# Kernel optimization log

Hardware: AMD Instinct MI355X
Metric: run time of the kernel (lower is better)

Reference implementation:

```python
import jax, jax.numpy as jnp
import numpy as np
from jax import lax

LEAK = 0.2
GN_EPS = 1e-5
K_NEIGH = 16
GROUPS = 4


def knn_idx(coor_k, coor_q, k):
    # coor_k: [B,Nk,3], coor_q: [B,Nq,3] -> [B,Nq,k] indices of k nearest in coor_k
    d = (jnp.sum(coor_q * coor_q, -1, keepdims=True)
         - 2.0 * jnp.einsum('bqc,bkc->bqk', coor_q, coor_k)
         + jnp.sum(coor_k * coor_k, -1)[:, None, :])
    _, idx = lax.top_k(-d, k)
    return idx


def graph_feature(coor_q, x_q, coor_k, x_k, k):
    # coor_*: [B,3,N*]; x_q: [B,C,Nq]; x_k: [B,C,Nk] -> [B,2C,Nq,k]
    idx = knn_idx(lax.stop_gradient(coor_k).transpose(0, 2, 1),
                  lax.stop_gradient(coor_q).transpose(0, 2, 1), k)
    B = x_k.shape[0]
    x_k_t = x_k.transpose(0, 2, 1)                      # [B,Nk,C]
    b_idx = jnp.arange(B)[:, None, None]
    nb = x_k_t[b_idx, idx]                              # [B,Nq,k,C]
    nb = nb.transpose(0, 3, 1, 2)                       # [B,C,Nq,k]
    xq = x_q[:, :, :, None]                             # [B,C,Nq,1]
    return jnp.concatenate([nb - xq, jnp.broadcast_to(xq, nb.shape)], axis=1)


def conv_gn_lrelu_max(f, w, gamma, beta):
    # f: [B,Cin,N,k]; w: [Cout,Cin] -> [B,Cout,N] (max over k)
    y = jnp.einsum('oc,bcnk->bonk', w, f)
    B, C, N, Kk = y.shape
    g = y.reshape(B, GROUPS, C // GROUPS, N, Kk)
    mu = g.mean((2, 3, 4), keepdims=True)
    var = g.var((2, 3, 4), keepdims=True)
    g = (g - mu) * lax.rsqrt(var + GN_EPS)
    y = g.reshape(B, C, N, Kk) * gamma[None, :, None, None] + beta[None, :, None, None]
    y = jnp.where(y >= 0, y, LEAK * y)
    return y.max(axis=-1)


def fps(xyz, n):
    # xyz: [B,N,3] -> [B,n] int32 (furthest point sampling, start at index 0)
    B, N, _ = xyz.shape
    d0 = jnp.sum((xyz - xyz[:, :1]) ** 2, -1)           # dist to point 0
    def body(dist, _):
        idx = jnp.argmax(dist, -1)                       # [B]
        nxt = jnp.take_along_axis(xyz, idx[:, None, None], 1)
        dist = jnp.minimum(dist, jnp.sum((xyz - nxt) ** 2, -1))
        return dist, idx
    _, idxs = lax.scan(body, d0, None, length=n - 1)     # [n-1,B]
    first = jnp.zeros((1, B), idxs.dtype)
    return jnp.concatenate([first, idxs], 0).T           # [B,n]


def fps_downsample(coor, x, n):
    # coor: [B,3,N], x: [B,C,N] -> ([B,3,n], [B,C,n])
    idx = fps(lax.stop_gradient(coor).transpose(0, 2, 1), n)
    comb = jnp.concatenate([coor, x], axis=1)            # [B,3+C,N]
    b_idx = jnp.arange(coor.shape[0])[:, None]
    new = comb.transpose(0, 2, 1)[b_idx, idx].transpose(0, 2, 1)
    return new[:, :3], new[:, 3:]


def setup_inputs() -> dict:
    key = jax.random.key(0)
    ks = jax.random.split(key, 16)
    s = 0.1
    return {
        'x': jax.random.normal(ks[0], (32, 2048, 3), jnp.float32),
        'w_in': jax.random.normal(ks[1], (8, 3), jnp.float32) * s,
        'b_in': jnp.zeros((8,), jnp.float32),
        'w1': jax.random.normal(ks[2], (32, 16), jnp.float32) * s,
        'g1': jnp.ones((32,), jnp.float32), 'be1': jnp.zeros((32,), jnp.float32),
        'w2': jax.random.normal(ks[3], (64, 64), jnp.float32) * s,
        'g2': jnp.ones((64,), jnp.float32), 'be2': jnp.zeros((64,), jnp.float32),
        'w3': jax.random.normal(ks[4], (64, 128), jnp.float32) * s,
        'g3': jnp.ones((64,), jnp.float32), 'be3': jnp.zeros((64,), jnp.float32),
        'w4': jax.random.normal(ks[5], (256, 128), jnp.float32) * s,
        'g4': jnp.ones((256,), jnp.float32), 'be4': jnp.zeros((256,), jnp.float32),
        'num0': 512,
        'num1': 128,
    }


def reference(x, w_in, b_in, w1, g1, be1, w2, g2, be2, w3, g3, be3, w4, g4, be4, num0, num1):
    coor = x.transpose(0, 2, 1)                          # [B,3,N]
    f = jnp.einsum('oc,bcn->bon', w_in, coor) + b_in[None, :, None]  # input_trans
    f = graph_feature(coor, f, coor, f, K_NEIGH)         # [B,16,N,k]
    f = conv_gn_lrelu_max(f, w1, g1, be1)                # [B,32,N]
    coor_q, f_q = fps_downsample(coor, f, num0)
    f = graph_feature(coor_q, f_q, coor, f, K_NEIGH)     # [B,64,num0,k]
    f = conv_gn_lrelu_max(f, w2, g2, be2)                # [B,64,num0]
    coor = coor_q
    f = graph_feature(coor, f, coor, f, K_NEIGH)         # [B,128,num0,k]
    f = conv_gn_lrelu_max(f, w3, g3, be3)                # [B,64,num0]
    coor_q, f_q = fps_downsample(coor, f, num1)
    f = graph_feature(coor_q, f_q, coor, f, K_NEIGH)     # [B,128,num1,k]
    f = conv_gn_lrelu_max(f, w4, g4, be4)                # [B,256,num1]
    coor = coor_q
    return coor.transpose(0, 2, 1), f.transpose(0, 2, 1)  # [B,num1,3], [B,num1,256]
```

## Files before the change

kernel.cpp:

```cpp
#include <hip/hip_runtime.h>

#define BB 32
#define NPTS0 2048
#define KNB 16
#define KC 256

constexpr int ilog2c(int n){ int l=0; while(n>1){ n>>=1; ++l; } return l; }

static __device__ __forceinline__ float sq3(float a, float b, float c){
  return __fadd_rn(__fadd_rn(__fmul_rn(a,a),__fmul_rn(b,b)),__fmul_rn(c,c));
}

template<int CTRL, int RM>
static __device__ __forceinline__ float dpp_maxf(float v){
  int s = __builtin_amdgcn_update_dpp(__float_as_int(v), __float_as_int(v), CTRL, RM, 0xF, false);
  return fmaxf(v, __int_as_float(s));
}
template<int CTRL, int RM>
static __device__ __forceinline__ unsigned dpp_minu(unsigned v){
  unsigned s = (unsigned)__builtin_amdgcn_update_dpp((int)v, (int)v, CTRL, RM, 0xF, false);
  return s < v ? s : v;
}

static __device__ __forceinline__ void proj_body(const float* __restrict__ x,
    const float* __restrict__ w, const float* __restrict__ bias, float* __restrict__ f0,
    int blk)
{
  int gid = blk*256 + threadIdx.x;
  if (gid >= BB*NPTS0) return;
  float x0 = x[gid*3+0], x1 = x[gid*3+1], x2 = x[gid*3+2];
  #pragma unroll
  for (int o = 0; o < 8; ++o){
    float acc = __fmul_rn(w[o*3+0], x0);
    acc = __fmaf_rn(w[o*3+1], x1, acc);
    acc = __fmaf_rn(w[o*3+2], x2, acc);
    f0[gid*8+o] = __fadd_rn(acc, bias[o]);
  }
}

#define KDECL(I) float th##I = __builtin_inff(); int ti##I = 0;
#define KINS(I,J) if (th##I < th##J){ float tv=th##I; th##I=th##J; th##J=tv; \
                                      int tj=ti##I; ti##I=ti##J; ti##J=tj; }
#define KCASCADE KINS(15,14) KINS(14,13) KINS(13,12) KINS(12,11) KINS(11,10) \
  KINS(10,9) KINS(9,8) KINS(8,7) KINS(7,6) KINS(6,5) KINS(5,4) KINS(4,3) \
  KINS(3,2) KINS(2,1) KINS(1,0)
#define KST(I) pd[base+I] = th##I; pi[base+I] = (unsigned char)ti##I;
#define MST(I) oidx[obase+I] = ti##I;

static __device__ __forceinline__ void knn_part_body(const float* __restrict__ qpts,
    const float* __restrict__ kpts, int Nq, int Nk, int nkc,
    float* __restrict__ pd, unsigned char* __restrict__ pi,
    int b, int qcb, int kc, float4* kk4)
{
  int tid = threadIdx.x;
  {
    int j = kc*KC + tid;
    float a = kpts[(b*Nk+j)*3+0];
    float c = kpts[(b*Nk+j)*3+1];
    float d = kpts[(b*Nk+j)*3+2];
    kk4[tid] = make_float4(a, c, d, sq3(a,c,d));
  }
  __syncthreads();
  int q = qcb*256 + tid;
  if (q >= Nq) return;
  float qx = qpts[(b*Nq+q)*3+0], qy = qpts[(b*Nq+q)*3+1], qz = qpts[(b*Nq+q)*3+2];
  float qq = sq3(qx,qy,qz);
  KDECL(0) KDECL(1) KDECL(2) KDECL(3) KDECL(4) KDECL(5) KDECL(6) KDECL(7)
  KDECL(8) KDECL(9) KDECL(10) KDECL(11) KDECL(12) KDECL(13) KDECL(14) KDECL(15)
  for (int j=0;j<KC;j++){
    float4 k4 = kk4[j];
    float dot = __fmul_rn(qx,k4.x);
    dot = __fmaf_rn(qy,k4.y,dot);
    dot = __fmaf_rn(qz,k4.z,dot);
    float d = __fadd_rn(__fsub_rn(qq, __fmul_rn(2.0f,dot)), k4.w);
    if (d < th15){
      th15 = d; ti15 = j;
      KCASCADE
    }
  }
  size_t base = ((size_t)(b*Nq+q)*nkc + kc)*KNB;
  KST(0) KST(1) KST(2) KST(3) KST(4) KST(5) KST(6) KST(7)
  KST(8) KST(9) KST(10) KST(11) KST(12) KST(13) KST(14) KST(15)
}

static __device__ __forceinline__ void knn_merge_body(const float* __restrict__ pd,
    const unsigned char* __restrict__ pi, int Nq, int nkc, int* __restrict__ oidx,
    int blk)
{
  int gid = blk*256 + threadIdx.x;
  if (gid >= BB*Nq) return;
  KDECL(0) KDECL(1) KDECL(2) KDECL(3) KDECL(4) KDECL(5) KDECL(6) KDECL(7)
  KDECL(8) KDECL(9) KDECL(10) KDECL(11) KDECL(12) KDECL(13) KDECL(14) KDECL(15)
  size_t base = (size_t)gid*nkc*KNB;
  for (int kc=0;kc<nkc;kc++){
    size_t cb = base + (size_t)kc*KNB;
    for (int i=0;i<KNB;i++){
      float d = pd[cb+i];
      if (d >= th15) break;
      int j = kc*KC + (int)pi[cb+i];
      th15 = d; ti15 = j;
      KCASCADE
    }
  }
  int obase = gid*KNB;
  MST(0) MST(1) MST(2) MST(3) MST(4) MST(5) MST(6) MST(7)
  MST(8) MST(9) MST(10) MST(11) MST(12) MST(13) MST(14) MST(15)
}

#define FPS_LOAD(T) float px##T, py##T, pz##T, d##T; { int i_=T*256+tid; \
  px##T=P[i_*3+0]; py##T=P[i_*3+1]; pz##T=P[i_*3+2]; \
  float dx_=__fsub_rn(px##T,c0x), dy_=__fsub_rn(py##T,c0y), dz_=__fsub_rn(pz##T,c0z); \
  d##T=sq3(dx_,dy_,dz_); bm=fmaxf(bm,d##T); }
#define FPS_MATCH(T) if (d##T == m_w) ci = (unsigned)(T*256 + tid);
#define FPS_OWN(T) if ((idx_w>>8) == T##u){ cx=px##T; cy=py##T; cz=pz##T; }
#define FPS_UPD(T) { float dx_=__fsub_rn(px##T,sx), dy_=__fsub_rn(py##T,sy), dz_=__fsub_rn(pz##T,sz); \
  float nd_=sq3(dx_,dy_,dz_); d##T=fminf(d##T,nd_); nbm=fmaxf(nbm,d##T); }

#define FPS_REDUCE_AND_PICK \
    float v = bm; \
    v = dpp_maxf<0x111, 0xF>(v); \
    v = dpp_maxf<0x112, 0xF>(v); \
    v = dpp_maxf<0x114, 0xF>(v); \
    v = dpp_maxf<0x118, 0xF>(v); \
    v = dpp_maxf<0x142, 0xA>(v); \
    v = dpp_maxf<0x143, 0xC>(v); \
    float m_w = __int_as_float(__builtin_amdgcn_readlane(__float_as_int(v), 63)); \
    unsigned ci = 0xFFFFFFFFu;

#define FPS_MIN_AND_MERGE \
    ci = dpp_minu<0x111, 0xF>(ci); \
    ci = dpp_minu<0x112, 0xF>(ci); \
    ci = dpp_minu<0x114, 0xF>(ci); \
    ci = dpp_minu<0x118, 0xF>(ci); \
    ci = dpp_minu<0x142, 0xA>(ci); \
    ci = dpp_minu<0x143, 0xC>(ci); \
    unsigned idx_w = (unsigned)__builtin_amdgcn_readlane((int)ci, 63); \
    int par = s & 1;

#define FPS_CROSSWAVE \
    __syncthreads(); \
    float4 q0 = *(const float4*)&swp[par][0][0]; float z0 = swp[par][0][4]; \
    float4 q1 = *(const float4*)&swp[par][1][0]; float z1 = swp[par][1][4]; \
    float4 q2 = *(const float4*)&swp[par][2][0]; float z2 = swp[par][2][4]; \
    float4 q3 = *(const float4*)&swp[par][3][0]; float z3 = swp[par][3][4]; \
    float mm = q0.x; unsigned mi = __float_as_uint(q0.y); \
    float sx = q0.z, sy = q0.w, sz = z0; \
    if (q1.x > mm || (q1.x == mm && __float_as_uint(q1.y) < mi)){ \
      mm = q1.x; mi = __float_as_uint(q1.y); sx = q1.z; sy = q1.w; sz = z1; } \
    if (q2.x > mm || (q2.x == mm && __float_as_uint(q2.y) < mi)){ \
      mm = q2.x; mi = __float_as_uint(q2.y); sx = q2.z; sy = q2.w; sz = z2; } \
    if (q3.x > mm || (q3.x == mm && __float_as_uint(q3.y) < mi)){ \
      mm = q3.x; mi = __float_as_uint(q3.y); sx = q3.z; sy = q3.w; sz = z3; } \
    if (tid == 0) oibuf[s] = (int)mi;

static __device__ __forceinline__ void fps8_body(const float* __restrict__ pts,
    int S, int* __restrict__ oidx, int b, char* smraw)
{
  float (*swp)[4][8] = reinterpret_cast<float(*)[4][8]>(smraw);
  int* oibuf = reinterpret_cast<int*>(smraw + 256);
  int tid = threadIdx.x, wid = tid >> 6;
  const float* P = pts + (size_t)b*2048*3;
  float c0x = P[0], c0y = P[1], c0z = P[2];
  float bm = -1.0f;
  FPS_LOAD(0) FPS_LOAD(1) FPS_LOAD(2) FPS_LOAD(3)
  FPS_LOAD(4) FPS_LOAD(5) FPS_LOAD(6) FPS_LOAD(7)
  if (tid == 0) oibuf[0] = 0;
  for (int s=1; s<S; ++s){
    FPS_REDUCE_AND_PICK
    FPS_MATCH(7) FPS_MATCH(6) FPS_MATCH(5) FPS_MATCH(4)
    FPS_MATCH(3) FPS_MATCH(2) FPS_MATCH(1) FPS_MATCH(0)
    FPS_MIN_AND_MERGE
    if (tid == (int)(idx_w & 255u)){
      float cx = px0, cy = py0, cz = pz0;
      FPS_OWN(1) FPS_OWN(2) FPS_OWN(3) FPS_OWN(4) FPS_OWN(5) FPS_OWN(6) FPS_OWN(7)
      float4* wp = (float4*)&swp[par][wid][0];
      *wp = make_float4(m_w, __uint_as_float(idx_w), cx, cy);
      swp[par][wid][4] = cz;
    }
    FPS_CROSSWAVE
    float nbm = -1.0f;
    FPS_UPD(0) FPS_UPD(1) FPS_UPD(2) FPS_UPD(3)
    FPS_UPD(4) FPS_UPD(5) FPS_UPD(6) FPS_UPD(7)
    bm = nbm;
  }
  __syncthreads();
  for (int s2 = tid; s2 < S; s2 += 256) oidx[b*S + s2] = oibuf[s2];
}

static __device__ __forceinline__ void fps2_body(const float* __restrict__ pts,
    int S, int* __restrict__ oidx, int b, char* smraw)
{
  float (*swp)[4][8] = reinterpret_cast<float(*)[4][8]>(smraw);
  int* oibuf = reinterpret_cast<int*>(smraw + 256);
  int tid = threadIdx.x, wid = tid >> 6;
  const float* P = pts + (size_t)b*512*3;
  float c0x = P[0], c0y = P[1], c0z = P[2];
  float bm = -1.0f;
  FPS_LOAD(0) FPS_LOAD(1)
  if (tid == 0) oibuf[0] = 0;
  for (int s=1; s<S; ++s){
    FPS_REDUCE_AND_PICK
    FPS_MATCH(1) FPS_MATCH(0)
    FPS_MIN_AND_MERGE
    if (tid == (int)(idx_w & 255u)){
      float cx = px0, cy = py0, cz = pz0;
      FPS_OWN(1)
      float4* wp = (float4*)&swp[par][wid][0];
      *wp = make_float4(m_w, __uint_as_float(idx_w), cx, cy);
      swp[par][wid][4] = cz;
    }
    FPS_CROSSWAVE
    float nbm = -1.0f;
    FPS_UPD(0) FPS_UPD(1)
    bm = nbm;
  }
  __syncthreads();
  for (int s2 = tid; s2 < S; s2 += 256) oidx[b*S + s2] = oibuf[s2];
}

__global__ __launch_bounds__(256) void fused1_kernel(const float* __restrict__ x,
    const float* __restrict__ w_in, const float* __restrict__ b_in,
    float* __restrict__ f0, float* __restrict__ pd1, unsigned char* __restrict__ pi1,
    int* __restrict__ fidx0)
{
  __shared__ __align__(16) char sm[4096];
  int bid = blockIdx.x;
  if (bid < 32){
    __builtin_amdgcn_s_setprio(3);
    fps8_body(x, 512, fidx0, bid, sm);
  } else if (bid < 32+2048){
    int r = bid - 32;
    int b = r & 31; int rest = r >> 5;
    knn_part_body(x, x, 2048, 2048, 8, pd1, pi1, b, rest & 7, rest >> 3, (float4*)sm);
  } else {
    proj_body(x, w_in, b_in, f0, bid - 2080);
  }
}

__global__ __launch_bounds__(256) void fused2_kernel(const float* __restrict__ coorq1,
    const float* __restrict__ x,
    float* __restrict__ pd2, unsigned char* __restrict__ pi2,
    float* __restrict__ pd3, unsigned char* __restrict__ pi3,
    int* __restrict__ fidx1,
    const float* __restrict__ pd1, const unsigned char* __restrict__ pi1,
    int* __restrict__ idx1)
{
  __shared__ __align__(16) char sm[4096];
  int bid = blockIdx.x;
  if (bid < 32){
    __builtin_amdgcn_s_setprio(3);
    fps2_body(coorq1, 128, fidx1, bid, sm);
  } else if (bid < 32+512){
    int r = bid - 32;
    int b = r & 31; int rest = r >> 5;
    knn_part_body(coorq1, x, 512, 2048, 8, pd2, pi2, b, rest & 1, rest >> 1, (float4*)sm);
  } else if (bid < 32+512+128){
    int r = bid - 544;
    int b = r & 31; int rest = r >> 5;
    knn_part_body(coorq1, coorq1, 512, 512, 2, pd3, pi3, b, rest & 1, rest >> 1, (float4*)sm);
  } else {
    knn_merge_body(pd1, pi1, 2048, 8, idx1, bid - 672);
  }
}

__global__ __launch_bounds__(256) void knn_part_kernel(const float* __restrict__ qpts,
    const float* __restrict__ kpts, int Nq, int Nk,
    float* __restrict__ pd, unsigned char* __restrict__ pi)
{
  __shared__ __align__(16) float4 kk4[KC];
  knn_part_body(qpts, kpts, Nq, Nk, gridDim.z, pd, pi,
                blockIdx.x, blockIdx.y, blockIdx.z, kk4);
}

__global__ __launch_bounds__(256) void knn_merge_kernel(const float* __restrict__ pd,
    const unsigned char* __restrict__ pi, int Nq, int nkc, int* __restrict__ oidx)
{
  knn_merge_body(pd, pi, Nq, nkc, oidx, blockIdx.x);
}

template<int C, int O, bool DIFF>
static __device__ __forceinline__ void gemv_body(const float* __restrict__ fin,
    const float* __restrict__ W, float* __restrict__ out, int Npts, int blk)
{
  constexpr int NT = O/8;
  constexpr int LNT = ilog2c(NT);
  int gid = blk*256 + threadIdx.x;
  if (gid >= BB*Npts*NT) return;
  int tile = gid & (NT-1);
  int pn = gid >> LNT;
  const float* frow = fin + pn*C;
  float f[C];
  #pragma unroll
  for (int c=0;c<C;c++) f[c] = frow[c];
  float acc[8];
  const float* wbase = W + (tile*8)*(2*C);
  #pragma unroll
  for (int oo=0;oo<8;oo++){
    const float* wrow = wbase + oo*(2*C);
    float a = 0.f;
    #pragma unroll
    for (int c=0;c<C;c++){
      float wv = DIFF ? __fsub_rn(wrow[C+c], wrow[c]) : wrow[c];
      a = __fmaf_rn(wv, f[c], a);
    }
    acc[oo] = a;
  }
  float* orow = out + pn*O + tile*8;
  #pragma unroll
  for (int oo=0;oo<8;oo++) orow[oo] = acc[oo];
}

template<int C, int O>
__global__ __launch_bounds__(256) void gemv_dual_kernel(const float* __restrict__ finA,
    const float* __restrict__ finB, const float* __restrict__ W,
    float* __restrict__ outA, float* __restrict__ outB,
    int NptsA, int NptsB, int nAblk)
{
  int bid = blockIdx.x;
  if (bid < nAblk) gemv_body<C,O,false>(finA, W, outA, NptsA, bid);
  else             gemv_body<C,O,true >(finB, W, outB, NptsB, bid - nAblk);
}

template<int O>
__global__ __launch_bounds__(256) void stats2_kernel(const float* __restrict__ A,
    const float* __restrict__ Bq, const int* __restrict__ idx, int Nq, int Nk,
    double* __restrict__ part)
{
  constexpr int O4 = O/4;
  int b = blockIdx.x, split = blockIdx.y, nsplit = gridDim.y;
  int qlen = Nq / nsplit, q0 = split*qlen;
  int tid = threadIdx.x;
  int pairs = qlen * KNB;
  double s1[4] = {0.0,0.0,0.0,0.0};
  double s2[4] = {0.0,0.0,0.0,0.0};
  for (int p = tid; p < pairs; p += 256){
    int q = q0 + (p >> 4);
    int kk = p & 15;
    int j = idx[(b*Nq+q)*KNB + kk];
    const float* arow = A + (size_t)(b*Nk+j)*O;
    const float* brow = Bq + (size_t)(b*Nq+q)*O;
    #pragma unroll
    for (int g=0; g<4; ++g){
      float cs1 = 0.f, cs2 = 0.f;
      #pragma unroll
      for (int c=0; c<O4; c+=4){
        float4 a4 = *(const float4*)(arow + g*O4 + c);
        float4 b4 = *(const float4*)(brow + g*O4 + c);
        float y0 = a4.x+b4.x, y1 = a4.y+b4.y, y2 = a4.z+b4.z, y3 = a4.w+b4.w;
        cs1 += ((y0+y1)+(y2+y3));
        cs2 = fmaf(y0,y0,cs2); cs2 = fmaf(y1,y1,cs2);
        cs2 = fmaf(y2,y2,cs2); cs2 = fmaf(y3,y3,cs2);
      }
      s1[g] += (double)cs1;
      s2[g] += (double)cs2;
    }
  }
  #pragma unroll
  for (int m=32;m>0;m>>=1){
    #pragma unroll
    for (int g=0; g<4; ++g){
      s1[g] += __shfl_down(s1[g], m);
      s2[g] += __shfl_down(s2[g], m);
    }
  }
  __shared__ double sh[4][8];
  int lane = tid & 63, w = tid >> 6;
  if (lane == 0){
    #pragma unroll
    for (int g=0; g<4; ++g){ sh[w][g*2] = s1[g]; sh[w][g*2+1] = s2[g]; }
  }
  __syncthreads();
  if (tid == 0){
    #pragma unroll
    for (int g=0; g<4; ++g){
      double t1 = (sh[0][g*2]+sh[1][g*2]) + (sh[2][g*2]+sh[3][g*2]);
      double t2 = (sh[0][g*2+1]+sh[1][g*2+1]) + (sh[2][g*2+1]+sh[3][g*2+1]);
      int pi = (b*4+g)*nsplit + split;
      part[pi*2] = t1; part[pi*2+1] = t2;
    }
  }
}

template<int O>
__global__ __launch_bounds__(256) void final_kernel(const float* __restrict__ A,
    const float* __restrict__ Bq, const int* __restrict__ idx,
    const double* __restrict__ part, int nsplit, double cnt,
    const float* __restrict__ gamma, const float* __restrict__ beta,
    float* __restrict__ fout, int Nq, int Nk)
{
  constexpr int LO = ilog2c(O);
  constexpr int LO4 = ilog2c(O/4);
  __shared__ float smu[4], srs[4];
  int b = blockIdx.y;
  if (threadIdx.x < 4){
    int g = threadIdx.x;
    int t0 = b*4+g;
    double s1=0.0, s2=0.0;
    for (int i=0;i<nsplit;i++){ s1 += part[(t0*nsplit+i)*2]; s2 += part[(t0*nsplit+i)*2+1]; }
    double mean = s1/cnt;
    double var = s2/cnt - mean*mean;
    double rstd = 1.0 / sqrt(var + 1e-5);
    smu[g] = (float)mean;
    srs[g] = (float)rstd;
  }
  __syncthreads();
  int t = blockIdx.x*256 + threadIdx.x;
  if (t >= Nq*O) return;
  int o = t & (O-1);
  int q = t >> LO;
  int g = o >> LO4;
  float mu   = smu[g];
  float rstd = srs[g];
  float gam = gamma[o], bet = beta[o];
  float bq = Bq[(b*Nq+q)*O + o];
  const int* ip = idx + (b*Nq+q)*KNB;
  float m = -__builtin_inff();
  #pragma unroll
  for (int kk=0;kk<KNB;kk++){
    int j = ip[kk];
    float y = A[(b*Nk+j)*O + o] + bq;
    float yn = __fmul_rn(__fsub_rn(y, mu), rstd);
    float yv = __fadd_rn(__fmul_rn(yn, gam), bet);
    float l = yv >= 0.f ? yv : 0.2f*yv;
    m = fmaxf(m, l);
  }
  fout[(b*Nq+q)*O + o] = m;
}

__global__ __launch_bounds__(256) void gatherc_kernel(const int* __restrict__ fidx,
    const float* __restrict__ pts, float* __restrict__ cq, int Nin, int Nout)
{
  int gid = blockIdx.x*256 + threadIdx.x;
  if (gid >= BB*Nout) return;
  int b = gid / Nout;
  int i = gid - b*Nout;
  int src = fidx[b*Nout + i];
  #pragma unroll
  for (int c=0;c<3;c++) cq[gid*3+c] = pts[(b*Nin+src)*3+c];
}

template<int C>
__global__ __launch_bounds__(256) void gatherf_kernel(const int* __restrict__ fidx,
    const float* __restrict__ fin, float* __restrict__ fq, int Nin, int Nout)
{
  int gid = blockIdx.x*256 + threadIdx.x;
  if (gid >= BB*Nout) return;
  int b = gid / Nout;
  int i = gid - b*Nout;
  int src = fidx[b*Nout + i];
  #pragma unroll
  for (int c=0;c<C;c++) fq[gid*C+c] = fin[(b*Nin+src)*C+c];
}

extern "C" void kernel_launch(void* const* d_in, const int* in_sizes, int n_in,
                              void* d_out, int out_size, void* d_ws, size_t ws_size,
                              hipStream_t stream)
{
  (void)in_sizes; (void)n_in; (void)out_size; (void)ws_size;
  const float* x    = (const float*)d_in[0];
  const float* w_in = (const float*)d_in[1];
  const float* b_in = (const float*)d_in[2];
  const float* w1 = (const float*)d_in[3];
  const float* g1 = (const float*)d_in[4];
  const float* be1= (const float*)d_in[5];
  const float* w2 = (const float*)d_in[6];
  const float* g2 = (const float*)d_in[7];
  const float* be2= (const float*)d_in[8];
  const float* w3 = (const float*)d_in[9];
  const float* g3 = (const float*)d_in[10];
  const float* be3= (const float*)d_in[11];
  const float* w4 = (const float*)d_in[12];
  const float* g4 = (const float*)d_in[13];
  const float* be4= (const float*)d_in[14];

  float* out = (float*)d_out;
  float* coor_out = out;
  float* f_out = out + BB*128*3;

  char* ws = (char*)d_ws;
  size_t off = 0;
  auto alloc = [&](size_t bytes)->void*{ void* p = ws + off; off += (bytes + 255) & ~(size_t)255; return p; };

  float* f0     = (float*)alloc((size_t)BB*2048*8*4);
  int*   idx1   = (int*)  alloc((size_t)BB*2048*16*4);
  float* f1     = (float*)alloc((size_t)BB*2048*32*4);
  double* part  = (double*)alloc((size_t)BB*4*8*2*8);
  int*   fidx0  = (int*)  alloc((size_t)BB*512*4);
  float* coorq1 = (float*)alloc((size_t)BB*512*3*4);
  float* fq1    = (float*)alloc((size_t)BB*512*32*4);
  int*   idx2   = (int*)  alloc((size_t)BB*512*16*4);
  float* f2     = (float*)alloc((size_t)BB*512*64*4);
  int*   idx3   = (int*)  alloc((size_t)BB*512*16*4);
  float* f3     = (float*)alloc((size_t)BB*512*64*4);
  int*   fidx1  = (int*)  alloc((size_t)BB*128*4);
  float* fq2    = (float*)alloc((size_t)BB*128*64*4);
  int*   idx4   = (int*)  alloc((size_t)BB*128*16*4);
  float* pd2          = (float*)alloc((size_t)BB*512*8*KNB*4);
  unsigned char* pi2  = (unsigned char*)alloc((size_t)BB*512*8*KNB);
  float* pd3          = (float*)alloc((size_t)BB*512*2*KNB*4);
  unsigned char* pi3  = (unsigned char*)alloc((size_t)BB*512*2*KNB);
  float* pd4          = (float*)alloc((size_t)BB*128*2*KNB*4);
  unsigned char* pi4  = (unsigned char*)alloc((size_t)BB*128*2*KNB);

  char* U = (char*)alloc((size_t)48<<20);
  float* pd1         = (float*)U;
  unsigned char* pi1 = (unsigned char*)(U + ((size_t)34<<20));
  float* A  = (float*)U;
  float* Bq = (float*)(U + ((size_t)20<<20));

  auto cdiv = [](int a, int b){ return (a+b-1)/b; };

  fused1_kernel<<<2336,256,0,stream>>>(x, w_in, b_in, f0, pd1, pi1, fidx0);

  gatherc_kernel<<<cdiv(BB*512,256),256,0,stream>>>(fidx0, x, coorq1, 2048, 512);

  fused2_kernel<<<928,256,0,stream>>>(coorq1, x, pd2, pi2, pd3, pi3, fidx1,
                                      pd1, pi1, idx1);

  gemv_dual_kernel<8,32><<<2048,256,0,stream>>>(f0, f0, w1, A, Bq, 2048, 2048, 1024);
  stats2_kernel<32><<<dim3(BB,8),256,0,stream>>>(A, Bq, idx1, 2048, 2048, part);
  final_kernel<32><<<dim3(cdiv(2048*32,256),BB),256,0,stream>>>(A, Bq, idx1, part, 8,
      8.0*2048*16, g1, be1, f1, 2048, 2048);
  gatherf_kernel<32><<<cdiv(BB*512,256),256,0,stream>>>(fidx0, f1, fq1, 2048, 512);

  knn_merge_kernel<<<cdiv(BB*512,256),256,0,stream>>>(pd2, pi2, 512, 8, idx2);
  knn_merge_kernel<<<cdiv(BB*512,256),256,0,stream>>>(pd3, pi3, 512, 2, idx3);

  gatherc_kernel<<<cdiv(BB*128,256),256,0,stream>>>(fidx1, coorq1, coor_out, 512, 128);
  knn_part_kernel<<<dim3(BB,1,2),256,0,stream>>>(coor_out, coorq1, 128, 512, pd4, pi4);
  knn_merge_kernel<<<cdiv(BB*128,256),256,0,stream>>>(pd4, pi4, 128, 2, idx4);

  gemv_dual_kernel<32,64><<<2560,256,0,stream>>>(f1, fq1, w2, A, Bq, 2048, 512, 2048);
  stats2_kernel<64><<<dim3(BB,8),256,0,stream>>>(A, Bq, idx2, 512, 2048, part);
  final_kernel<64><<<dim3(cdiv(512*64,256),BB),256,0,stream>>>(A, Bq, idx2, part, 8,
      16.0*512*16, g2, be2, f2, 512, 2048);

  gemv_dual_kernel<64,64><<<1024,256,0,stream>>>(f2, f2, w3, A, Bq, 512, 512, 512);
  stats2_kernel<64><<<dim3(BB,8),256,0,stream>>>(A, Bq, idx3, 512, 512, part);
  final_kernel<64><<<dim3(cdiv(512*64,256),BB),256,0,stream>>>(A, Bq, idx3, part, 8,
      16.0*512*16, g3, be3, f3, 512, 512);

  gatherf_kernel<64><<<cdiv(BB*128,256),256,0,stream>>>(fidx1, f3, fq2, 512, 128);
  gemv_dual_kernel<64,256><<<2560,256,0,stream>>>(f3, fq2, w4, A, Bq, 512, 128, 2048);
  stats2_kernel<256><<<dim3(BB,8),256,0,stream>>>(A, Bq, idx4, 128, 512, part);
  final_kernel<256><<<dim3(cdiv(128*256,256),BB),256,0,stream>>>(A, Bq, idx4, part, 8,
      64.0*128*16, g4, be4, f_out, 128, 512);
}
```

Before: 1.337 ms.

## Fuse more stages into multi-role kernels and widen first kNN chunks

```diff
diff --git a/kernel.cpp b/kernel.cpp
--- a/kernel.cpp
+++ b/kernel.cpp
@@ -44,13 +44,54 @@
 #define KCASCADE KINS(15,14) KINS(14,13) KINS(13,12) KINS(12,11) KINS(11,10) \
   KINS(10,9) KINS(9,8) KINS(8,7) KINS(7,6) KINS(6,5) KINS(5,4) KINS(4,3) \
   KINS(3,2) KINS(2,1) KINS(1,0)
+#define KALLDECL KDECL(0) KDECL(1) KDECL(2) KDECL(3) KDECL(4) KDECL(5) KDECL(6) KDECL(7) \
+  KDECL(8) KDECL(9) KDECL(10) KDECL(11) KDECL(12) KDECL(13) KDECL(14) KDECL(15)
 #define KST(I) pd[base+I] = th##I; pi[base+I] = (unsigned char)ti##I;
+#define KST16(I) pd[base+I] = th##I; pi[base+I] = (unsigned short)ti##I;
 #define MST(I) oidx[obase+I] = ti##I;
+
+static __device__ __forceinline__ void knn_part512_body(const float* __restrict__ qpts,
+    const float* __restrict__ kpts, int Nq, int Nk, int nkc,
+    float* __restrict__ pd, unsigned short* __restrict__ pi,
+    int b, int qcb, int kc, float4* kk4)
+{
+  int tid = threadIdx.x;
+  int q = qcb*256 + tid;
+  float qx = qpts[(b*Nq+q)*3+0], qy = qpts[(b*Nq+q)*3+1], qz = qpts[(b*Nq+q)*3+2];
+  float qq = sq3(qx,qy,qz);
+  KALLDECL
+  #pragma unroll
+  for (int half=0; half<2; ++half){
+    __syncthreads();
+    {
+      int j = kc*512 + half*256 + tid;
+      float a = kpts[(b*Nk+j)*3+0];
+      float c = kpts[(b*Nk+j)*3+1];
+      float dd = kpts[(b*Nk+j)*3+2];
+      kk4[tid] = make_float4(a, c, dd, sq3(a,c,dd));
+    }
+    __syncthreads();
+    for (int j=0;j<KC;j++){
+      float4 k4 = kk4[j];
+      float dot = __fmul_rn(qx,k4.x);
+      dot = __fmaf_rn(qy,k4.y,dot);
+      dot = __fmaf_rn(qz,k4.z,dot);
+      float d = __fadd_rn(__fsub_rn(qq, __fmul_rn(2.0f,dot)), k4.w);
+      if (d < th15){
+        th15 = d; ti15 = half*256 + j;
+        KCASCADE
+      }
+    }
+  }
+  size_t base = ((size_t)(b*Nq+q)*nkc + kc)*KNB;
+  KST16(0) KST16(1) KST16(2) KST16(3) KST16(4) KST16(5) KST16(6) KST16(7)
+  KST16(8) KST16(9) KST16(10) KST16(11) KST16(12) KST16(13) KST16(14) KST16(15)
+}
 
 static __device__ __forceinline__ void knn_part_body(const float* __restrict__ qpts,
     const float* __restrict__ kpts, int Nq, int Nk, int nkc,
     float* __restrict__ pd, unsigned char* __restrict__ pi,
-    int b, int qcb, int kc, float4* kk4)
+    int b, int qcb, int kc, float4* kk4, const int* __restrict__ qidx, int NinQ)
 {
   int tid = threadIdx.x;
   {
@@ -63,10 +104,10 @@
   __syncthreads();
   int q = qcb*256 + tid;
   if (q >= Nq) return;
-  float qx = qpts[(b*Nq+q)*3+0], qy = qpts[(b*Nq+q)*3+1], qz = qpts[(b*Nq+q)*3+2];
+  int qrow = qidx ? (b*NinQ + qidx[b*Nq+q]) : (b*Nq+q);
+  float qx = qpts[qrow*3+0], qy = qpts[qrow*3+1], qz = qpts[qrow*3+2];
   float qq = sq3(qx,qy,qz);
-  KDECL(0) KDECL(1) KDECL(2) KDECL(3) KDECL(4) KDECL(5) KDECL(6) KDECL(7)
-  KDECL(8) KDECL(9) KDECL(10) KDECL(11) KDECL(12) KDECL(13) KDECL(14) KDECL(15)
+  KALLDECL
   for (int j=0;j<KC;j++){
     float4 k4 = kk4[j];
     float dot = __fmul_rn(qx,k4.x);
@@ -89,8 +130,7 @@
 {
   int gid = blk*256 + threadIdx.x;
   if (gid >= BB*Nq) return;
-  KDECL(0) KDECL(1) KDECL(2) KDECL(3) KDECL(4) KDECL(5) KDECL(6) KDECL(7)
-  KDECL(8) KDECL(9) KDECL(10) KDECL(11) KDECL(12) KDECL(13) KDECL(14) KDECL(15)
+  KALLDECL
   size_t base = (size_t)gid*nkc*KNB;
   for (int kc=0;kc<nkc;kc++){
     size_t cb = base + (size_t)kc*KNB;
@@ -98,6 +138,29 @@
       float d = pd[cb+i];
       if (d >= th15) break;
       int j = kc*KC + (int)pi[cb+i];
+      th15 = d; ti15 = j;
+      KCASCADE
+    }
+  }
+  int obase = gid*KNB;
+  MST(0) MST(1) MST(2) MST(3) MST(4) MST(5) MST(6) MST(7)
+  MST(8) MST(9) MST(10) MST(11) MST(12) MST(13) MST(14) MST(15)
+}
+
+static __device__ __forceinline__ void knn_merge512_body(const float* __restrict__ pd,
+    const unsigned short* __restrict__ pi, int Nq, int nkc, int* __restrict__ oidx,
+    int blk)
+{
+  int gid = blk*256 + threadIdx.x;
+  if (gid >= BB*Nq) return;
+  KALLDECL
+  size_t base = (size_t)gid*nkc*KNB;
+  for (int kc=0;kc<nkc;kc++){
+    size_t cb = base + (size_t)kc*KNB;
+    for (int i=0;i<KNB;i++){
+      float d = pd[cb+i];
+      if (d >= th15) break;
+      int j = kc*512 + (int)pi[cb+i];
       th15 = d; ti15 = j;
       KCASCADE
     }
@@ -218,66 +281,6 @@
   for (int s2 = tid; s2 < S; s2 += 256) oidx[b*S + s2] = oibuf[s2];
 }
 
-__global__ __launch_bounds__(256) void fused1_kernel(const float* __restrict__ x,
-    const float* __restrict__ w_in, const float* __restrict__ b_in,
-    float* __restrict__ f0, float* __restrict__ pd1, unsigned char* __restrict__ pi1,
-    int* __restrict__ fidx0)
-{
-  __shared__ __align__(16) char sm[4096];
-  int bid = blockIdx.x;
-  if (bid < 32){
-    __builtin_amdgcn_s_setprio(3);
-    fps8_body(x, 512, fidx0, bid, sm);
-  } else if (bid < 32+2048){
-    int r = bid - 32;
-    int b = r & 31; int rest = r >> 5;
-    knn_part_body(x, x, 2048, 2048, 8, pd1, pi1, b, rest & 7, rest >> 3, (float4*)sm);
-  } else {
-    proj_body(x, w_in, b_in, f0, bid - 2080);
-  }
-}
-
-__global__ __launch_bounds__(256) void fused2_kernel(const float* __restrict__ coorq1,
-    const float* __restrict__ x,
-    float* __restrict__ pd2, unsigned char* __restrict__ pi2,
-    float* __restrict__ pd3, unsigned char* __restrict__ pi3,
-    int* __restrict__ fidx1,
-    const float* __restrict__ pd1, const unsigned char* __restrict__ pi1,
-    int* __restrict__ idx1)
-{
-  __shared__ __align__(16) char sm[4096];
-  int bid = blockIdx.x;
-  if (bid < 32){
-    __builtin_amdgcn_s_setprio(3);
-    fps2_body(coorq1, 128, fidx1, bid, sm);
-  } else if (bid < 32+512){
-    int r = bid - 32;
-    int b = r & 31; int rest = r >> 5;
-    knn_part_body(coorq1, x, 512, 2048, 8, pd2, pi2, b, rest & 1, rest >> 1, (float4*)sm);
-  } else if (bid < 32+512+128){
-    int r = bid - 544;
-    int b = r & 31; int rest = r >> 5;
-    knn_part_body(coorq1, coorq1, 512, 512, 2, pd3, pi3, b, rest & 1, rest >> 1, (float4*)sm);
-  } else {
-    knn_merge_body(pd1, pi1, 2048, 8, idx1, bid - 672);
-  }
-}
-
-__global__ __launch_bounds__(256) void knn_part_kernel(const float* __restrict__ qpts,
-    const float* __restrict__ kpts, int Nq, int Nk,
-    float* __restrict__ pd, unsigned char* __restrict__ pi)
-{
-  __shared__ __align__(16) float4 kk4[KC];
-  knn_part_body(qpts, kpts, Nq, Nk, gridDim.z, pd, pi,
-                blockIdx.x, blockIdx.y, blockIdx.z, kk4);
-}
-
-__global__ __launch_bounds__(256) void knn_merge_kernel(const float* __restrict__ pd,
-    const unsigned char* __restrict__ pi, int Nq, int nkc, int* __restrict__ oidx)
-{
-  knn_merge_body(pd, pi, Nq, nkc, oidx, blockIdx.x);
-}
-
 template<int C, int O, bool DIFF>
 static __device__ __forceinline__ void gemv_body(const float* __restrict__ fin,
     const float* __restrict__ W, float* __restrict__ out, int Npts, int blk)
@@ -288,7 +291,7 @@
   if (gid >= BB*Npts*NT) return;
   int tile = gid & (NT-1);
   int pn = gid >> LNT;
-  const float* frow = fin + pn*C;
+  const float* frow = fin + (size_t)pn*C;
   float f[C];
   #pragma unroll
   for (int c=0;c<C;c++) f[c] = frow[c];
@@ -305,29 +308,64 @@
     }
     acc[oo] = a;
   }
-  float* orow = out + pn*O + tile*8;
+  float* orow = out + (size_t)pn*O + tile*8;
   #pragma unroll
   for (int oo=0;oo<8;oo++) orow[oo] = acc[oo];
 }
 
-template<int C, int O>
+template<int C, int O, int LNB>
+static __device__ __forceinline__ void gemv_bodyBind(const float* __restrict__ fin,
+    const float* __restrict__ W, float* __restrict__ out, int blk,
+    const int* __restrict__ gidx, int NinB)
+{
+  constexpr int NT = O/8;
+  constexpr int LNT = ilog2c(NT);
+  int gid = blk*256 + threadIdx.x;
+  if (gid >= BB*(1<<LNB)*NT) return;
+  int tile = gid & (NT-1);
+  int pn = gid >> LNT;
+  int b = pn >> LNB;
+  int src = gidx[pn];
+  const float* frow = fin + (size_t)(b*NinB + src)*C;
+  float f[C];
+  #pragma unroll
+  for (int c=0;c<C;c++) f[c] = frow[c];
+  float acc[8];
+  const float* wbase = W + (tile*8)*(2*C);
+  #pragma unroll
+  for (int oo=0;oo<8;oo++){
+    const float* wrow = wbase + oo*(2*C);
+    float a = 0.f;
+    #pragma unroll
+    for (int c=0;c<C;c++){
+      float wv = __fsub_rn(wrow[C+c], wrow[c]);
+      a = __fmaf_rn(wv, f[c], a);
+    }
+    acc[oo] = a;
+  }
+  float* orow = out + (size_t)pn*O + tile*8;
+  #pragma unroll
+  for (int oo=0;oo<8;oo++) orow[oo] = acc[oo];
+}
+
+template<int C, int O, int LNB, bool BIND>
 __global__ __launch_bounds__(256) void gemv_dual_kernel(const float* __restrict__ finA,
     const float* __restrict__ finB, const float* __restrict__ W,
     float* __restrict__ outA, float* __restrict__ outB,
-    int NptsA, int NptsB, int nAblk)
+    int NptsA, int NptsB, int nAblk, const int* __restrict__ gidxB, int NinB)
 {
   int bid = blockIdx.x;
   if (bid < nAblk) gemv_body<C,O,false>(finA, W, outA, NptsA, bid);
-  else             gemv_body<C,O,true >(finB, W, outB, NptsB, bid - nAblk);
+  else if constexpr (BIND) gemv_bodyBind<C,O,LNB>(finB, W, outB, bid-nAblk, gidxB, NinB);
+  else gemv_body<C,O,true>(finB, W, outB, NptsB, bid-nAblk);
 }
 
 template<int O>
-__global__ __launch_bounds__(256) void stats2_kernel(const float* __restrict__ A,
+static __device__ __forceinline__ void stats2_body(const float* __restrict__ A,
     const float* __restrict__ Bq, const int* __restrict__ idx, int Nq, int Nk,
-    double* __restrict__ part)
+    double* __restrict__ part, int b, int split, int nsplit, double* sh )
 {
   constexpr int O4 = O/4;
-  int b = blockIdx.x, split = blockIdx.y, nsplit = gridDim.y;
   int qlen = Nq / nsplit, q0 = split*qlen;
   int tid = threadIdx.x;
   int pairs = qlen * KNB;
@@ -363,22 +401,30 @@
       s2[g] += __shfl_down(s2[g], m);
     }
   }
-  __shared__ double sh[4][8];
   int lane = tid & 63, w = tid >> 6;
   if (lane == 0){
     #pragma unroll
-    for (int g=0; g<4; ++g){ sh[w][g*2] = s1[g]; sh[w][g*2+1] = s2[g]; }
+    for (int g=0; g<4; ++g){ sh[w*8+g*2] = s1[g]; sh[w*8+g*2+1] = s2[g]; }
   }
   __syncthreads();
   if (tid == 0){
     #pragma unroll
     for (int g=0; g<4; ++g){
-      double t1 = (sh[0][g*2]+sh[1][g*2]) + (sh[2][g*2]+sh[3][g*2]);
-      double t2 = (sh[0][g*2+1]+sh[1][g*2+1]) + (sh[2][g*2+1]+sh[3][g*2+1]);
+      double t1 = (sh[0*8+g*2]+sh[1*8+g*2]) + (sh[2*8+g*2]+sh[3*8+g*2]);
+      double t2 = (sh[0*8+g*2+1]+sh[1*8+g*2+1]) + (sh[2*8+g*2+1]+sh[3*8+g*2+1]);
       int pi = (b*4+g)*nsplit + split;
       part[pi*2] = t1; part[pi*2+1] = t2;
     }
   }
+}
+
+template<int O>
+__global__ __launch_bounds__(256) void stats2_kernel(const float* __restrict__ A,
+    const float* __restrict__ Bq, const int* __restrict__ idx, int Nq, int Nk,
+    double* __restrict__ part)
+{
+  __shared__ double sh[32];
+  stats2_body<O>(A, Bq, idx, Nq, Nk, part, blockIdx.x, blockIdx.y, gridDim.y, sh);
 }
 
 template<int O>
@@ -427,10 +473,10 @@
   fout[(b*Nq+q)*O + o] = m;
 }
 
-__global__ __launch_bounds__(256) void gatherc_kernel(const int* __restrict__ fidx,
-    const float* __restrict__ pts, float* __restrict__ cq, int Nin, int Nout)
-{
-  int gid = blockIdx.x*256 + threadIdx.x;
+static __device__ __forceinline__ void gatherc_body(const int* __restrict__ fidx,
+    const float* __restrict__ pts, float* __restrict__ cq, int Nin, int Nout, int blk)
+{
+  int gid = blk*256 + threadIdx.x;
   if (gid >= BB*Nout) return;
   int b = gid / Nout;
   int i = gid - b*Nout;
@@ -439,17 +485,102 @@
   for (int c=0;c<3;c++) cq[gid*3+c] = pts[(b*Nin+src)*3+c];
 }
 
-template<int C>
-__global__ __launch_bounds__(256) void gatherf_kernel(const int* __restrict__ fidx,
-    const float* __restrict__ fin, float* __restrict__ fq, int Nin, int Nout)
-{
-  int gid = blockIdx.x*256 + threadIdx.x;
-  if (gid >= BB*Nout) return;
-  int b = gid / Nout;
-  int i = gid - b*Nout;
-  int src = fidx[b*Nout + i];
-  #pragma unroll
-  for (int c=0;c<C;c++) fq[gid*C+c] = fin[(b*Nin+src)*C+c];
+__global__ __launch_bounds__(256) void gatherc_kernel(const int* __restrict__ fidx,
+    const float* __restrict__ pts, float* __restrict__ cq, int Nin, int Nout)
+{
+  gatherc_body(fidx, pts, cq, Nin, Nout, blockIdx.x);
+}
+
+__global__ __launch_bounds__(256) void fused1_kernel(const float* __restrict__ x,
+    const float* __restrict__ w_in, const float* __restrict__ b_in,
+    float* __restrict__ f0, float* __restrict__ pd1, unsigned short* __restrict__ pi1,
+    int* __restrict__ fidx0)
+{
+  __shared__ __align__(16) char sm[4096];
+  int bid = blockIdx.x;
+  if (bid < 32){
+    __builtin_amdgcn_s_setprio(3);
+    fps8_body(x, 512, fidx0, bid, sm);
+  } else if (bid < 32+1024){
+    int r = bid - 32;
+    int b = r & 31; int rest = r >> 5;
+    knn_part512_body(x, x, 2048, 2048, 4, pd1, pi1, b, rest & 7, rest >> 3, (float4*)sm);
+  } else {
+    proj_body(x, w_in, b_in, f0, bid - 1056);
+  }
+}
+
+__global__ __launch_bounds__(256) void fused2_kernel(const float* __restrict__ coorq1,
+    const float* __restrict__ x,
+    float* __restrict__ pd2, unsigned char* __restrict__ pi2,
+    float* __restrict__ pd3, unsigned char* __restrict__ pi3,
+    int* __restrict__ fidx1,
+    const float* __restrict__ pd1, const unsigned short* __restrict__ pi1,
+    int* __restrict__ idx1,
+    const float* __restrict__ f0, const float* __restrict__ w1,
+    float* __restrict__ A1, float* __restrict__ B1)
+{
+  __shared__ __align__(16) char sm[4096];
+  int bid = blockIdx.x;
+  if (bid < 32){
+    __builtin_amdgcn_s_setprio(3);
+    fps2_body(coorq1, 128, fidx1, bid, sm);
+  } else if (bid < 32+512){
+    int r = bid - 32;
+    int b = r & 31; int rest = r >> 5;
+    knn_part_body(coorq1, x, 512, 2048, 8, pd2, pi2, b, rest & 1, rest >> 1,
+                  (float4*)sm, nullptr, 0);
+  } else if (bid < 32+512+128){
+    int r = bid - 544;
+    int b = r & 31; int rest = r >> 5;
+    knn_part_body(coorq1, coorq1, 512, 512, 2, pd3, pi3, b, rest & 1, rest >> 1,
+                  (float4*)sm, nullptr, 0);
+  } else if (bid < 928){
+    knn_merge512_body(pd1, pi1, 2048, 4, idx1, bid - 672);
+  } else if (bid < 1952){
+    gemv_body<8,32,false>(f0, w1, A1, 2048, bid - 928);
+  } else {
+    gemv_body<8,32,true>(f0, w1, B1, 2048, bid - 1952);
+  }
+}
+
+__global__ __launch_bounds__(256) void fused3_kernel(
+    const float* __restrict__ A1, const float* __restrict__ B1,
+    const int* __restrict__ idx1, double* __restrict__ part,
+    const float* __restrict__ pd2, const unsigned char* __restrict__ pi2, int* __restrict__ idx2,
+    const float* __restrict__ pd3, const unsigned char* __restrict__ pi3, int* __restrict__ idx3,
+    const float* __restrict__ coorq1, const int* __restrict__ fidx1,
+    float* __restrict__ pd4, unsigned char* __restrict__ pi4,
+    float* __restrict__ coor_out)
+{
+  __shared__ __align__(16) char sm[4096];
+  int bid = blockIdx.x;
+  if (bid < 256){
+    stats2_body<32>(A1, B1, idx1, 2048, 2048, part, bid >> 3, bid & 7, 8, (double*)sm);
+  } else if (bid < 320){
+    knn_merge_body(pd2, pi2, 512, 8, idx2, bid - 256);
+  } else if (bid < 384){
+    knn_merge_body(pd3, pi3, 512, 2, idx3, bid - 320);
+  } else if (bid < 448){
+    int r = bid - 384;
+    int b = r & 31; int kc = r >> 5;
+    knn_part_body(coorq1, coorq1, 128, 512, 2, pd4, pi4, b, 0, kc,
+                  (float4*)sm, fidx1, 512);
+  } else {
+    gatherc_body(fidx1, coorq1, coor_out, 512, 128, bid - 448);
+  }
+}
+
+__global__ __launch_bounds__(256) void fused4_kernel(const float* __restrict__ f1,
+    const float* __restrict__ w2, float* __restrict__ A, float* __restrict__ Bq,
+    const int* __restrict__ fidx0,
+    const float* __restrict__ pd4, const unsigned char* __restrict__ pi4,
+    int* __restrict__ idx4)
+{
+  int bid = blockIdx.x;
+  if (bid < 2048) gemv_body<32,64,false>(f1, w2, A, 2048, bid);
+  else if (bid < 2560) gemv_bodyBind<32,64,9>(f1, w2, Bq, bid - 2048, fidx0, 2048);
+  else knn_merge_body(pd4, pi4, 128, 2, idx4, bid - 2560);
 }
 
 extern "C" void kernel_launch(void* const* d_in, const int* in_sizes, int n_in,
@@ -487,13 +618,11 @@
   double* part  = (double*)alloc((size_t)BB*4*8*2*8);
   int*   fidx0  = (int*)  alloc((size_t)BB*512*4);
   float* coorq1 = (float*)alloc((size_t)BB*512*3*4);
-  float* fq1    = (float*)alloc((size_t)BB*512*32*4);
   int*   idx2   = (int*)  alloc((size_t)BB*512*16*4);
   float* f2     = (float*)alloc((size_t)BB*512*64*4);
   int*   idx3   = (int*)  alloc((size_t)BB*512*16*4);
   float* f3     = (float*)alloc((size_t)BB*512*64*4);
   int*   fidx1  = (int*)  alloc((size_t)BB*128*4);
-  float* fq2    = (float*)alloc((size_t)BB*128*64*4);
   int*   idx4   = (int*)  alloc((size_t)BB*128*16*4);
   float* pd2          = (float*)alloc((size_t)BB*512*8*KNB*4);
   unsigned char* pi2  = (unsigned char*)alloc((size_t)BB*512*8*KNB);
@@ -502,46 +631,35 @@
   float* pd4          = (float*)alloc((size_t)BB*128*2*KNB*4);
   unsigned char* pi4  = (unsigned char*)alloc((size_t)BB*128*2*KNB);
 
-  char* U = (char*)alloc((size_t)48<<20);
-  float* pd1         = (float*)U;
-  unsigned char* pi1 = (unsigned char*)(U + ((size_t)34<<20));
+  char* U = (char*)alloc((size_t)40<<20);
+  float* pd1          = (float*)U;
+  unsigned short* pi1 = (unsigned short*)(U + ((size_t)16<<20));
+  float* A1 = (float*)(U + ((size_t)24<<20));
+  float* B1 = (float*)(U + ((size_t)32<<20));
   float* A  = (float*)U;
   float* Bq = (float*)(U + ((size_t)20<<20));
 
   auto cdiv = [](int a, int b){ return (a+b-1)/b; };
 
-  fused1_kernel<<<2336,256,0,stream>>>(x, w_in, b_in, f0, pd1, pi1, fidx0);
-
+  fused1_kernel<<<1312,256,0,stream>>>(x, w_in, b_in, f0, pd1, pi1, fidx0);
   gatherc_kernel<<<cdiv(BB*512,256),256,0,stream>>>(fidx0, x, coorq1, 2048, 512);
-
-  fused2_kernel<<<928,256,0,stream>>>(coorq1, x, pd2, pi2, pd3, pi3, fidx1,
-                                      pd1, pi1, idx1);
-
-  gemv_dual_kernel<8,32><<<2048,256,0,stream>>>(f0, f0, w1, A, Bq, 2048, 2048, 1024);
-  stats2_kernel<32><<<dim3(BB,8),256,0,stream>>>(A, Bq, idx1, 2048, 2048, part);
-  final_kernel<32><<<dim3(cdiv(2048*32,256),BB),256,0,stream>>>(A, Bq, idx1, part, 8,
+  fused2_kernel<<<2976,256,0,stream>>>(coorq1, x, pd2, pi2, pd3, pi3, fidx1,
+                                       pd1, pi1, idx1, f0, w1, A1, B1);
+  fused3_kernel<<<464,256,0,stream>>>(A1, B1, idx1, part, pd2, pi2, idx2,
+                                      pd3, pi3, idx3, coorq1, fidx1, pd4, pi4, coor_out);
+  final_kernel<32><<<dim3(cdiv(2048*32,256),BB),256,0,stream>>>(A1, B1, idx1, part, 8,
       8.0*2048*16, g1, be1, f1, 2048, 2048);
-  gatherf_kernel<32><<<cdiv(BB*512,256),256,0,stream>>>(fidx0, f1, fq1, 2048, 512);
-
-  knn_merge_kernel<<<cdiv(BB*512,256),256,0,stream>>>(pd2, pi2, 512, 8, idx2);
-  knn_merge_kernel<<<cdiv(BB*512,256),256,0,stream>>>(pd3, pi3, 512, 2, idx3);
-
-  gatherc_kernel<<<cdiv(BB*128,256),256,0,stream>>>(fidx1, coorq1, coor_out, 512, 128);
-  knn_part_kernel<<<dim3(BB,1,2),256,0,stream>>>(coor_out, coorq1, 128, 512, pd4, pi4);
-  knn_merge_kernel<<<cdiv(BB*128,256),256,0,stream>>>(pd4, pi4, 128, 2, idx4);
-
-  gemv_dual_kernel<32,64><<<2560,256,0,stream>>>(f1, fq1, w2, A, Bq, 2048, 512, 2048);
+  fused4_kernel<<<2576,256,0,stream>>>(f1, w2, A, Bq, fidx0, pd4, pi4, idx4);
   stats2_kernel<64><<<dim3(BB,8),256,0,stream>>>(A, Bq, idx2, 512, 2048, part);
   final_kernel<64><<<dim3(cdiv(512*64,256),BB),256,0,stream>>>(A, Bq, idx2, part, 8,
       16.0*512*16, g2, be2, f2, 512, 2048);
-
-  gemv_dual_kernel<64,64><<<1024,256,0,stream>>>(f2, f2, w3, A, Bq, 512, 512, 512);
+  gemv_dual_kernel<64,64,0,false><<<1024,256,0,stream>>>(f2, f2, w3, A, Bq,
+      512, 512, 512, nullptr, 0);
   stats2_kernel<64><<<dim3(BB,8),256,0,stream>>>(A, Bq, idx3, 512, 512, part);
   final_kernel<64><<<dim3(cdiv(512*64,256),BB),256,0,stream>>>(A, Bq, idx3, part, 8,
       16.0*512*16, g3, be3, f3, 512, 512);
-
-  gatherf_kernel<64><<<cdiv(BB*128,256),256,0,stream>>>(fidx1, f3, fq2, 512, 128);
-  gemv_dual_kernel<64,256><<<2560,256,0,stream>>>(f3, fq2, w4, A, Bq, 512, 128, 2048);
+  gemv_dual_kernel<64,256,7,true><<<2560,256,0,stream>>>(f3, f3, w4, A, Bq,
+      512, 128, 2048, fidx1, 512);
   stats2_kernel<256><<<dim3(BB,8),256,0,stream>>>(A, Bq, idx4, 128, 512, part);
   final_kernel<256><<<dim3(cdiv(128*256,256),BB),256,0,stream>>>(A, Bq, idx4, part, 8,
       64.0*128*16, g4, be4, f_out, 128, 512);
```

After: 1.218 ms. 1.1x faster.
